# Kernel tuning notes

Hardware: AMD Instinct MI355X
Metric: run time of the kernel (lower is better)

The kernel has to match this reference:

```python
import jax, jax.numpy as jnp
import numpy as np


def setup_inputs() -> dict:
    key = jax.random.key(0)
    k1, k2, k3 = jax.random.split(key, 3)
    B, H, S, D = 4, 16, 1024, 64
    return {
        "query": jax.random.normal(k1, (B, H, S, D), dtype=jnp.float32),
        "key": jax.random.normal(k2, (B, H, D, S), dtype=jnp.float32),  # pre-transposed K
        "scale_factor": 8,  # sqrt(head_dim)
        "attention_mask": jnp.zeros((S, S), dtype=jnp.float32),
        "value": jax.random.normal(k3, (B, H, S, D), dtype=jnp.float32),
    }


def reference(query, key, scale_factor, attention_mask, value):
    # Batched equivalent of the per-(b,h) Python loop:
    # scores = Q @ K^T / scale + mask; probs = softmax(scores); out = probs @ V
    scores = jnp.matmul(query, key) / scale_factor  # [B,H,S,S]
    if attention_mask is not None:
        scores = scores + attention_mask  # broadcast [S,S] over [B,H,S,S]
    probs = jax.nn.softmax(scores, axis=-1)
    return jnp.matmul(probs, value)  # [B,H,S,D]
```

## Files before the change

kernel.cpp:

```cpp
#include <hip/hip_runtime.h>

#define BH  64
#define SEQ 1024
#define DIM 64
#define KT  64
#define NT  (SEQ / KT)

typedef __attribute__((ext_vector_type(8))) short  short8;
typedef __attribute__((ext_vector_type(4))) float  floatx4;

__device__ __forceinline__ ushort f2bf(float x) {
    union { float f; uint u; } v; v.f = x;
    uint r = v.u + 0x7FFFu + ((v.u >> 16) & 1u);
    return (ushort)(r >> 16);
}
__device__ __forceinline__ uint pack2(float lo, float hi) {
    return (uint)f2bf(lo) | ((uint)f2bf(hi) << 16);
}
__device__ __forceinline__ void gld_lds16(const void* g, void* l) {
    __builtin_amdgcn_global_load_lds(
        (const __attribute__((address_space(1))) unsigned int*)g,
        (__attribute__((address_space(3))) unsigned int*)l, 16, 0, 0);
}


__global__ __launch_bounds__(256) void prep_kv_kernel(
    const float* __restrict__ Kin,
    const float* __restrict__ Vin,
    ushort* __restrict__ Kbf, ushort* __restrict__ Vbf)
{
    __shared__ float tile[64][65];
    const int t    = threadIdx.x;
    const int head = blockIdx.y;
    const int s0   = blockIdx.x * 64;
    const int p    = t & 7;

    if (blockIdx.z == 0) {
        const float* ip = Kin + (size_t)head * DIM * SEQ;
#pragma unroll
        for (int i = 0; i < 4; ++i) {
            const int d = (t >> 4) + i * 16;
            const int c = (t & 15) * 4;
            float4 v = *(const float4*)(ip + (size_t)d * SEQ + s0 + c);
            tile[d][c]     = v.x; tile[d][c + 1] = v.y;
            tile[d][c + 2] = v.z; tile[d][c + 3] = v.w;
        }
        __syncthreads();
        char* op = (char*)(Kbf + (size_t)head * SEQ * DIM);
#pragma unroll
        for (int i = 0; i < 2; ++i) {
            const int s  = (t >> 3) + i * 32;
            const int dg = (p ^ (s & 7)) * 8;
            uint4 wv;
            wv.x = pack2(tile[dg + 0][s], tile[dg + 1][s]);
            wv.y = pack2(tile[dg + 2][s], tile[dg + 3][s]);
            wv.z = pack2(tile[dg + 4][s], tile[dg + 5][s]);
            wv.w = pack2(tile[dg + 6][s], tile[dg + 7][s]);
            *(uint4*)(op + (size_t)(s0 + s) * 128 + p * 16) = wv;
        }
    } else {
        const float* ip = Vin + (size_t)head * SEQ * DIM;
#pragma unroll
        for (int i = 0; i < 4; ++i) {
            const int ss = (t >> 4) + i * 16;
            const int c  = (t & 15) * 4;
            float4 v = *(const float4*)(ip + (size_t)(s0 + ss) * DIM + c);
            tile[ss][c]     = v.x; tile[ss][c + 1] = v.y;
            tile[ss][c + 2] = v.z; tile[ss][c + 3] = v.w;
        }
        __syncthreads();
        char* op = (char*)(Vbf + (size_t)head * SEQ * DIM) + (size_t)(s0 >> 6) * 8192;
#pragma unroll
        for (int i = 0; i < 2; ++i) {
            const int d  = (t >> 3) + i * 32;
            const int sg = (p ^ (d & 7)) * 8;
            uint4 wv;
            wv.x = pack2(tile[sg + 0][d], tile[sg + 1][d]);
            wv.y = pack2(tile[sg + 2][d], tile[sg + 3][d]);
            wv.z = pack2(tile[sg + 4][d], tile[sg + 5][d]);
            wv.w = pack2(tile[sg + 6][d], tile[sg + 7][d]);
            *(uint4*)(op + (size_t)d * 128 + p * 16) = wv;
        }
    }
}

__global__ __launch_bounds__(256, 4) void mha_mfma2_kernel(
    const float*  __restrict__ Q,
    const ushort* __restrict__ Kbf,
    const int*    __restrict__ scale_p,
    const float*  __restrict__ mask,
    const ushort* __restrict__ Vbf,
    float*        __restrict__ O)
{
    __shared__ __align__(16) ushort Ks0[KT * 64], Ks1[KT * 64];
    __shared__ __align__(16) ushort Vt0[DIM * 64], Vt1[DIM * 64];
    __shared__ __align__(16) ushort Ps[4 * 16 * 64];

    const int t    = threadIdx.x;
    const int lane = t & 63, w = t >> 6;
    const int li   = lane & 15, quad = lane >> 4;
    const int lx   = li & 7;
    const int bh   = blockIdx.x >> 4;
    const int q0   = (blockIdx.x & 15) * 64;

    const float inv_scale = 1.0f / (float)scale_p[0];

    {
        const float* Qg = Q + ((size_t)bh * SEQ + q0) * DIM;
        const int rr = t >> 4, cc = (t & 15) * 4;
#pragma unroll
        for (int i = 0; i < 4; ++i) {
            const int row = rr + 16 * i;
            float4 v = *(const float4*)(Qg + (size_t)row * DIM + cc);
            uint2 pw; pw.x = pack2(v.x, v.y); pw.y = pack2(v.z, v.w);
            *(uint2*)((char*)Ks0 + row * 128 + (((cc >> 3) ^ (row & 7)) * 16)
                      + (cc & 7) * 2) = pw;
        }
    }
    __syncthreads();
    const char* qrow = (const char*)Ks0 + (w * 16 + li) * 128;
    const short8 qa0 = *(const short8*)(qrow + ((quad ^ lx) * 16));
    const short8 qa1 = *(const short8*)(qrow + (((4 + quad) ^ lx) * 16));
    __syncthreads();

    floatx4 o[4] = {floatx4{0,0,0,0}, floatx4{0,0,0,0},
                    floatx4{0,0,0,0}, floatx4{0,0,0,0}};
    float l_r[4] = {0.f, 0.f, 0.f, 0.f};

    const char* KgH = (const char*)(Kbf + (size_t)bh * SEQ * DIM);
    const char* VgH = (const char*)(Vbf + (size_t)bh * SEQ * DIM);
    const int so = w * 2048 + lane * 16;
    char* ksd0 = (char*)Ks0 + w * 2048;
    char* ksd1 = (char*)Ks1 + w * 2048;
    char* vtd0 = (char*)Vt0 + w * 2048;
    char* vtd1 = (char*)Vt1 + w * 2048;
    char* psw  = (char*)Ps  + w * 2048;

    const float* mrow = mask + (size_t)(q0 + w * 16 + quad * 4) * SEQ + li;

    float mvc[16], mvn[16];
#pragma unroll
    for (int n = 0; n < 4; ++n)
#pragma unroll
        for (int r = 0; r < 4; ++r)
            mvc[n * 4 + r] = mrow[(size_t)r * SEQ + n * 16];
    gld_lds16(KgH + so,        ksd0);
    gld_lds16(KgH + so + 1024, ksd0 + 1024);
    gld_lds16(VgH + so,        vtd0);
    gld_lds16(VgH + so + 1024, vtd0 + 1024);
    __builtin_amdgcn_sched_barrier(0);

#pragma unroll 2
    for (int kt = 0; kt < NT; ++kt) {
        const int c = kt & 1;
        const char* ksb = c ? (const char*)Ks1 : (const char*)Ks0;
        const char* vtb = c ? (const char*)Vt1 : (const char*)Vt0;
        char* ksdN = c ? ksd0 : ksd1;
        char* vtdN = c ? vtd0 : vtd1;

        __builtin_amdgcn_s_barrier();

        const int kn = (kt + 1) & (NT - 1);
#pragma unroll
        for (int n = 0; n < 4; ++n)
#pragma unroll
            for (int r = 0; r < 4; ++r)
                mvn[n * 4 + r] = mrow[(size_t)r * SEQ + kn * KT + n * 16];
        {
            const char* kg = KgH + kn * 8192 + so;
            const char* vg = VgH + kn * 8192 + so;
            gld_lds16(kg,        ksdN);
            gld_lds16(kg + 1024, ksdN + 1024);
            gld_lds16(vg,        vtdN);
            gld_lds16(vg + 1024, vtdN + 1024);
        }
        __builtin_amdgcn_sched_barrier(0);
        asm volatile("s_waitcnt vmcnt(20)" ::: "memory");
        __builtin_amdgcn_sched_barrier(0);
        __builtin_amdgcn_s_barrier();

        floatx4 cfr[4] = {floatx4{0,0,0,0}, floatx4{0,0,0,0},
                          floatx4{0,0,0,0}, floatx4{0,0,0,0}};
        __builtin_amdgcn_s_setprio(1);
#pragma unroll
        for (int n = 0; n < 4; ++n) {
            const char* krow = ksb + (n * 16 + li) * 128;
            short8 b0 = *(const short8*)(krow + ((quad ^ lx) * 16));
            short8 b1 = *(const short8*)(krow + (((4 + quad) ^ lx) * 16));
            cfr[n] = __builtin_amdgcn_mfma_f32_16x16x32_bf16(qa0, b0, cfr[n], 0, 0, 0);
            cfr[n] = __builtin_amdgcn_mfma_f32_16x16x32_bf16(qa1, b1, cfr[n], 0, 0, 0);
        }
        __builtin_amdgcn_s_setprio(0);

#pragma unroll
        for (int n = 0; n < 4; ++n)
#pragma unroll
            for (int r = 0; r < 4; ++r) {
                float s = fminf(fmaf(cfr[n][r], inv_scale, mvc[n * 4 + r]), 80.f);
                float p = __expf(s);
                l_r[r] += p;
                const int row = quad * 4 + r, col = n * 16 + li;
                *(ushort*)(psw + row * 128 + (((col >> 3) ^ (row & 7)) * 16)
                           + (col & 7) * 2) = f2bf(p);
            }

        __builtin_amdgcn_s_setprio(1);
#pragma unroll
        for (int kk = 0; kk < 2; ++kk) {
            short8 a = *(const short8*)(psw + li * 128 + (((kk * 4 + quad) ^ lx) * 16));
#pragma unroll
            for (int n = 0; n < 4; ++n) {
                const char* vrow = vtb + (n * 16 + li) * 128;
                short8 b = *(const short8*)(vrow + (((kk * 4 + quad) ^ lx) * 16));
                o[n] = __builtin_amdgcn_mfma_f32_16x16x32_bf16(a, b, o[n], 0, 0, 0);
            }
        }
        __builtin_amdgcn_s_setprio(0);

#pragma unroll
        for (int j = 0; j < 16; ++j) mvc[j] = mvn[j];
    }

#pragma unroll
    for (int off = 1; off < 16; off <<= 1)
#pragma unroll
        for (int r = 0; r < 4; ++r)
            l_r[r] += __shfl_xor(l_r[r], off);

    float* Og = O + ((size_t)bh * SEQ + q0) * DIM;
#pragma unroll
    for (int r = 0; r < 4; ++r) {
        const float inv_l = 1.0f / l_r[r];
#pragma unroll
        for (int n = 0; n < 4; ++n)
            Og[(size_t)(w * 16 + quad * 4 + r) * DIM + n * 16 + li] = o[n][r] * inv_l;
    }
}

extern "C" void kernel_launch(void* const* d_in, const int* in_sizes, int n_in,
                              void* d_out, int out_size, void* d_ws, size_t ws_size,
                              hipStream_t stream) {
    const float* Q     = (const float*)d_in[0];
    const float* K     = (const float*)d_in[1];
    const int*   scale = (const int*)d_in[2];
    const float* mask  = (const float*)d_in[3];
    const float* V     = (const float*)d_in[4];
    float*       Out   = (float*)d_out;

    ushort* Kbf = (ushort*)d_ws;
    ushort* Vbf = Kbf + (size_t)BH * SEQ * DIM;

    prep_kv_kernel<<<dim3(SEQ / 64, BH, 2), 256, 0, stream>>>(K, V, Kbf, Vbf);
    mha_mfma2_kernel<<<dim3(BH * (SEQ / KT)), 256, 0, stream>>>(Q, Kbf, scale, mask, Vbf, Out);
}
```

Baseline: 136.3 us.

## Keep softmax probabilities in registers by computing transposed S and permuting V layout

Swaps the MFMA operands so the score tile comes out transposed, which lets each lane's exp values be packed straight into the A operand of the PV MFMA with no LDS round trip for P. The V prep kernel reorders its key groups to match this register layout, and mask loads become float4 vector loads along the key dimension. The row-sum reduction is reworked to match, and the wait count is lowered because fewer outstanding loads are issued. Bf16 rounding now uses a cheaper round-half-up perm-based pack, which changes rounding slightly on ties.

Measured after the change: 145.2 us. +6.6%, slower.

```diff
diff --git a/kernel.cpp b/kernel.cpp
--- a/kernel.cpp
+++ b/kernel.cpp
@@ -8,6 +8,7 @@
 
 typedef __attribute__((ext_vector_type(8))) short  short8;
 typedef __attribute__((ext_vector_type(4))) float  floatx4;
+typedef __attribute__((ext_vector_type(4))) uint   uintx4;
 
 __device__ __forceinline__ ushort f2bf(float x) {
     union { float f; uint u; } v; v.f = x;
@@ -16,6 +17,11 @@
 }
 __device__ __forceinline__ uint pack2(float lo, float hi) {
     return (uint)f2bf(lo) | ((uint)f2bf(hi) << 16);
+}
+__device__ __forceinline__ uint pk2(float lo, float hi) {
+    union { float f; uint u; } a, b; a.f = lo; b.f = hi;
+    uint au = a.u + 0x8000u, bu = b.u + 0x8000u;
+    return __builtin_amdgcn_perm(bu, au, 0x07060302);
 }
 __device__ __forceinline__ void gld_lds16(const void* g, void* l) {
     __builtin_amdgcn_global_load_lds(
@@ -73,12 +79,13 @@
 #pragma unroll
         for (int i = 0; i < 2; ++i) {
             const int d  = (t >> 3) + i * 32;
-            const int sg = (p ^ (d & 7)) * 8;
+            const int g  = p ^ (d & 7);
+            const int kb = ((g >> 2) * 32) + ((g & 3) * 4);
             uint4 wv;
-            wv.x = pack2(tile[sg + 0][d], tile[sg + 1][d]);
-            wv.y = pack2(tile[sg + 2][d], tile[sg + 3][d]);
-            wv.z = pack2(tile[sg + 4][d], tile[sg + 5][d]);
-            wv.w = pack2(tile[sg + 6][d], tile[sg + 7][d]);
+            wv.x = pack2(tile[kb +  0][d], tile[kb +  1][d]);
+            wv.y = pack2(tile[kb +  2][d], tile[kb +  3][d]);
+            wv.z = pack2(tile[kb + 16][d], tile[kb + 17][d]);
+            wv.w = pack2(tile[kb + 18][d], tile[kb + 19][d]);
             *(uint4*)(op + (size_t)d * 128 + p * 16) = wv;
         }
     }
@@ -94,7 +101,6 @@
 {
     __shared__ __align__(16) ushort Ks0[KT * 64], Ks1[KT * 64];
     __shared__ __align__(16) ushort Vt0[DIM * 64], Vt1[DIM * 64];
-    __shared__ __align__(16) ushort Ps[4 * 16 * 64];
 
     const int t    = threadIdx.x;
     const int lane = t & 63, w = t >> 6;
@@ -125,7 +131,7 @@
 
     floatx4 o[4] = {floatx4{0,0,0,0}, floatx4{0,0,0,0},
                     floatx4{0,0,0,0}, floatx4{0,0,0,0}};
-    float l_r[4] = {0.f, 0.f, 0.f, 0.f};
+    float l = 0.f;
 
     const char* KgH = (const char*)(Kbf + (size_t)bh * SEQ * DIM);
     const char* VgH = (const char*)(Vbf + (size_t)bh * SEQ * DIM);
@@ -134,16 +140,13 @@
     char* ksd1 = (char*)Ks1 + w * 2048;
     char* vtd0 = (char*)Vt0 + w * 2048;
     char* vtd1 = (char*)Vt1 + w * 2048;
-    char* psw  = (char*)Ps  + w * 2048;
-
-    const float* mrow = mask + (size_t)(q0 + w * 16 + quad * 4) * SEQ + li;
-
-    float mvc[16], mvn[16];
+
+    const float* mrow = mask + (size_t)(q0 + w * 16 + li) * SEQ + quad * 4;
+
+    float4 mvc[4], mvn[4];
 #pragma unroll
     for (int n = 0; n < 4; ++n)
-#pragma unroll
-        for (int r = 0; r < 4; ++r)
-            mvc[n * 4 + r] = mrow[(size_t)r * SEQ + n * 16];
+        mvc[n] = *(const float4*)(mrow + n * 16);
     gld_lds16(KgH + so,        ksd0);
     gld_lds16(KgH + so + 1024, ksd0 + 1024);
     gld_lds16(VgH + so,        vtd0);
@@ -163,9 +166,7 @@
         const int kn = (kt + 1) & (NT - 1);
 #pragma unroll
         for (int n = 0; n < 4; ++n)
-#pragma unroll
-            for (int r = 0; r < 4; ++r)
-                mvn[n * 4 + r] = mrow[(size_t)r * SEQ + kn * KT + n * 16];
+            mvn[n] = *(const float4*)(mrow + kn * KT + n * 16);
         {
             const char* kg = KgH + kn * 8192 + so;
             const char* vg = VgH + kn * 8192 + so;
@@ -175,7 +176,7 @@
             gld_lds16(vg + 1024, vtdN + 1024);
         }
         __builtin_amdgcn_sched_barrier(0);
-        asm volatile("s_waitcnt vmcnt(20)" ::: "memory");
+        asm volatile("s_waitcnt vmcnt(8)" ::: "memory");
         __builtin_amdgcn_sched_barrier(0);
         __builtin_amdgcn_s_barrier();
 
@@ -185,55 +186,58 @@
 #pragma unroll
         for (int n = 0; n < 4; ++n) {
             const char* krow = ksb + (n * 16 + li) * 128;
-            short8 b0 = *(const short8*)(krow + ((quad ^ lx) * 16));
-            short8 b1 = *(const short8*)(krow + (((4 + quad) ^ lx) * 16));
-            cfr[n] = __builtin_amdgcn_mfma_f32_16x16x32_bf16(qa0, b0, cfr[n], 0, 0, 0);
-            cfr[n] = __builtin_amdgcn_mfma_f32_16x16x32_bf16(qa1, b1, cfr[n], 0, 0, 0);
+            short8 kf0 = *(const short8*)(krow + ((quad ^ lx) * 16));
+            short8 kf1 = *(const short8*)(krow + (((4 + quad) ^ lx) * 16));
+            cfr[n] = __builtin_amdgcn_mfma_f32_16x16x32_bf16(kf0, qa0, cfr[n], 0, 0, 0);
+            cfr[n] = __builtin_amdgcn_mfma_f32_16x16x32_bf16(kf1, qa1, cfr[n], 0, 0, 0);
         }
         __builtin_amdgcn_s_setprio(0);
 
+        uint pw[8];
+#pragma unroll
+        for (int n = 0; n < 4; ++n) {
+            const float4 m4 = mvc[n];
+            float s0 = fminf(fmaf(cfr[n][0], inv_scale, m4.x), 80.f);
+            float s1 = fminf(fmaf(cfr[n][1], inv_scale, m4.y), 80.f);
+            float s2 = fminf(fmaf(cfr[n][2], inv_scale, m4.z), 80.f);
+            float s3 = fminf(fmaf(cfr[n][3], inv_scale, m4.w), 80.f);
+            float p0 = __expf(s0), p1 = __expf(s1);
+            float p2 = __expf(s2), p3 = __expf(s3);
+            l += ((p0 + p1) + (p2 + p3));
+            pw[n * 2]     = pk2(p0, p1);
+            pw[n * 2 + 1] = pk2(p2, p3);
+        }
+        const short8 pa0 = __builtin_bit_cast(short8, uintx4{pw[0], pw[1], pw[2], pw[3]});
+        const short8 pa1 = __builtin_bit_cast(short8, uintx4{pw[4], pw[5], pw[6], pw[7]});
+
+        __builtin_amdgcn_s_setprio(1);
+#pragma unroll
+        for (int n = 0; n < 4; ++n) {
+            const char* vrow = vtb + (n * 16 + li) * 128;
+            short8 b0 = *(const short8*)(vrow + ((quad ^ lx) * 16));
+            short8 b1 = *(const short8*)(vrow + (((4 + quad) ^ lx) * 16));
+            o[n] = __builtin_amdgcn_mfma_f32_16x16x32_bf16(pa0, b0, o[n], 0, 0, 0);
+            o[n] = __builtin_amdgcn_mfma_f32_16x16x32_bf16(pa1, b1, o[n], 0, 0, 0);
+        }
+        __builtin_amdgcn_s_setprio(0);
+
+#pragma unroll
+        for (int j = 0; j < 4; ++j) mvc[j] = mvn[j];
+    }
+
+    l += __shfl_xor(l, 16);
+    l += __shfl_xor(l, 32);
+    float linv[4];
+#pragma unroll
+    for (int r = 0; r < 4; ++r)
+        linv[r] = 1.0f / __shfl(l, quad * 4 + r);
+
+    float* Og = O + ((size_t)bh * SEQ + q0) * DIM;
+#pragma unroll
+    for (int r = 0; r < 4; ++r) {
 #pragma unroll
         for (int n = 0; n < 4; ++n)
-#pragma unroll
-            for (int r = 0; r < 4; ++r) {
-                float s = fminf(fmaf(cfr[n][r], inv_scale, mvc[n * 4 + r]), 80.f);
-                float p = __expf(s);
-                l_r[r] += p;
-                const int row = quad * 4 + r, col = n * 16 + li;
-                *(ushort*)(psw + row * 128 + (((col >> 3) ^ (row & 7)) * 16)
-                           + (col & 7) * 2) = f2bf(p);
-            }
-
-        __builtin_amdgcn_s_setprio(1);
-#pragma unroll
-        for (int kk = 0; kk < 2; ++kk) {
-            short8 a = *(const short8*)(psw + li * 128 + (((kk * 4 + quad) ^ lx) * 16));
-#pragma unroll
-            for (int n = 0; n < 4; ++n) {
-                const char* vrow = vtb + (n * 16 + li) * 128;
-                short8 b = *(const short8*)(vrow + (((kk * 4 + quad) ^ lx) * 16));
-                o[n] = __builtin_amdgcn_mfma_f32_16x16x32_bf16(a, b, o[n], 0, 0, 0);
-            }
-        }
-        __builtin_amdgcn_s_setprio(0);
-
-#pragma unroll
-        for (int j = 0; j < 16; ++j) mvc[j] = mvn[j];
-    }
-
-#pragma unroll
-    for (int off = 1; off < 16; off <<= 1)
-#pragma unroll
-        for (int r = 0; r < 4; ++r)
-            l_r[r] += __shfl_xor(l_r[r], off);
-
-    float* Og = O + ((size_t)bh * SEQ + q0) * DIM;
-#pragma unroll
-    for (int r = 0; r < 4; ++r) {
-        const float inv_l = 1.0f / l_r[r];
-#pragma unroll
-        for (int n = 0; n < 4; ++n)
-            Og[(size_t)(w * 16 + quad * 4 + r) * DIM + n * 16 + li] = o[n][r] * inv_l;
+            Og[(size_t)(w * 16 + quad * 4 + r) * DIM + n * 16 + li] = o[n][r] * linv[r];
     }
 }
 
```

## Split each key tile across two warps per query block with LDS reduction

Applied to the files above, without the earlier changes.

Doubles the block to 512 threads. Each pair of warps shares a 16-row query slice, and each warp of the pair handles half of every 64-key tile for both QK^T and PV. Partial outputs and row sums are combined through shared memory at the end. The aim is more waves in flight to hide latency and shorter per-warp critical paths. The cost is an extra LDS reduction, a final barrier, and fewer MFMAs per wave to amortize the per-tile synchronization.

Result: slower. 239.1 us (+75.4%).

```diff
diff --git a/kernel.cpp b/kernel.cpp
--- a/kernel.cpp
+++ b/kernel.cpp
@@ -84,7 +84,7 @@
     }
 }
 
-__global__ __launch_bounds__(256, 4) void mha_mfma2_kernel(
+__global__ __launch_bounds__(512, 8) void mha_mfma2_kernel(
     const float*  __restrict__ Q,
     const ushort* __restrict__ Kbf,
     const int*    __restrict__ scale_p,
@@ -92,12 +92,11 @@
     const ushort* __restrict__ Vbf,
     float*        __restrict__ O)
 {
-    __shared__ __align__(16) ushort Ks0[KT * 64], Ks1[KT * 64];
-    __shared__ __align__(16) ushort Vt0[DIM * 64], Vt1[DIM * 64];
-    __shared__ __align__(16) ushort Ps[4 * 16 * 64];
+    __shared__ __align__(16) char smem[40960];
 
     const int t    = threadIdx.x;
     const int lane = t & 63, w = t >> 6;
+    const int wq   = w >> 1, wk = w & 1;
     const int li   = lane & 15, quad = lane >> 4;
     const int lx   = li & 7;
     const int bh   = blockIdx.x >> 4;
@@ -109,16 +108,16 @@
         const float* Qg = Q + ((size_t)bh * SEQ + q0) * DIM;
         const int rr = t >> 4, cc = (t & 15) * 4;
 #pragma unroll
-        for (int i = 0; i < 4; ++i) {
-            const int row = rr + 16 * i;
+        for (int i = 0; i < 2; ++i) {
+            const int row = rr + 32 * i;
             float4 v = *(const float4*)(Qg + (size_t)row * DIM + cc);
             uint2 pw; pw.x = pack2(v.x, v.y); pw.y = pack2(v.z, v.w);
-            *(uint2*)((char*)Ks0 + row * 128 + (((cc >> 3) ^ (row & 7)) * 16)
+            *(uint2*)(smem + row * 128 + (((cc >> 3) ^ (row & 7)) * 16)
                       + (cc & 7) * 2) = pw;
         }
     }
     __syncthreads();
-    const char* qrow = (const char*)Ks0 + (w * 16 + li) * 128;
+    const char* qrow = smem + (wq * 16 + li) * 128;
     const short8 qa0 = *(const short8*)(qrow + ((quad ^ lx) * 16));
     const short8 qa1 = *(const short8*)(qrow + (((4 + quad) ^ lx) * 16));
     __syncthreads();
@@ -129,62 +128,49 @@
 
     const char* KgH = (const char*)(Kbf + (size_t)bh * SEQ * DIM);
     const char* VgH = (const char*)(Vbf + (size_t)bh * SEQ * DIM);
-    const int so = w * 2048 + lane * 16;
-    char* ksd0 = (char*)Ks0 + w * 2048;
-    char* ksd1 = (char*)Ks1 + w * 2048;
-    char* vtd0 = (char*)Vt0 + w * 2048;
-    char* vtd1 = (char*)Vt1 + w * 2048;
-    char* psw  = (char*)Ps  + w * 2048;
-
-    const float* mrow = mask + (size_t)(q0 + w * 16 + quad * 4) * SEQ + li;
-
-    float mvc[16], mvn[16];
-#pragma unroll
-    for (int n = 0; n < 4; ++n)
+    const int so = w * 1024 + lane * 16;
+    char* psw = smem + 32768 + w * 1024;
+
+    const float* mrow = mask + (size_t)(q0 + wq * 16 + quad * 4) * SEQ + wk * 32 + li;
+
+    float mvc[8], mvn[8];
+#pragma unroll
+    for (int n = 0; n < 2; ++n)
 #pragma unroll
         for (int r = 0; r < 4; ++r)
             mvc[n * 4 + r] = mrow[(size_t)r * SEQ + n * 16];
-    gld_lds16(KgH + so,        ksd0);
-    gld_lds16(KgH + so + 1024, ksd0 + 1024);
-    gld_lds16(VgH + so,        vtd0);
-    gld_lds16(VgH + so + 1024, vtd0 + 1024);
+    gld_lds16(KgH + so,         smem + w * 1024);
+    gld_lds16(VgH + so,         smem + 16384 + w * 1024);
     __builtin_amdgcn_sched_barrier(0);
 
 #pragma unroll 2
     for (int kt = 0; kt < NT; ++kt) {
         const int c = kt & 1;
-        const char* ksb = c ? (const char*)Ks1 : (const char*)Ks0;
-        const char* vtb = c ? (const char*)Vt1 : (const char*)Vt0;
-        char* ksdN = c ? ksd0 : ksd1;
-        char* vtdN = c ? vtd0 : vtd1;
+        const char* ksb = smem + (c ? 8192 : 0);
+        const char* vtb = smem + 16384 + (c ? 8192 : 0);
+        char* ksdN = smem + (c ? 0 : 8192) + w * 1024;
+        char* vtdN = smem + 16384 + (c ? 0 : 8192) + w * 1024;
 
         __builtin_amdgcn_s_barrier();
 
         const int kn = (kt + 1) & (NT - 1);
 #pragma unroll
-        for (int n = 0; n < 4; ++n)
+        for (int n = 0; n < 2; ++n)
 #pragma unroll
             for (int r = 0; r < 4; ++r)
                 mvn[n * 4 + r] = mrow[(size_t)r * SEQ + kn * KT + n * 16];
-        {
-            const char* kg = KgH + kn * 8192 + so;
-            const char* vg = VgH + kn * 8192 + so;
-            gld_lds16(kg,        ksdN);
-            gld_lds16(kg + 1024, ksdN + 1024);
-            gld_lds16(vg,        vtdN);
-            gld_lds16(vg + 1024, vtdN + 1024);
-        }
+        gld_lds16(KgH + kn * 8192 + so, ksdN);
+        gld_lds16(VgH + kn * 8192 + so, vtdN);
         __builtin_amdgcn_sched_barrier(0);
-        asm volatile("s_waitcnt vmcnt(20)" ::: "memory");
+        asm volatile("s_waitcnt vmcnt(10)" ::: "memory");
         __builtin_amdgcn_sched_barrier(0);
         __builtin_amdgcn_s_barrier();
 
-        floatx4 cfr[4] = {floatx4{0,0,0,0}, floatx4{0,0,0,0},
-                          floatx4{0,0,0,0}, floatx4{0,0,0,0}};
+        floatx4 cfr[2] = {floatx4{0,0,0,0}, floatx4{0,0,0,0}};
         __builtin_amdgcn_s_setprio(1);
 #pragma unroll
-        for (int n = 0; n < 4; ++n) {
-            const char* krow = ksb + (n * 16 + li) * 128;
+        for (int n = 0; n < 2; ++n) {
+            const char* krow = ksb + (wk * 32 + n * 16 + li) * 128;
             short8 b0 = *(const short8*)(krow + ((quad ^ lx) * 16));
             short8 b1 = *(const short8*)(krow + (((4 + quad) ^ lx) * 16));
             cfr[n] = __builtin_amdgcn_mfma_f32_16x16x32_bf16(qa0, b0, cfr[n], 0, 0, 0);
@@ -193,33 +179,35 @@
         __builtin_amdgcn_s_setprio(0);
 
 #pragma unroll
-        for (int n = 0; n < 4; ++n)
+        for (int n = 0; n < 2; ++n)
 #pragma unroll
             for (int r = 0; r < 4; ++r) {
                 float s = fminf(fmaf(cfr[n][r], inv_scale, mvc[n * 4 + r]), 80.f);
                 float p = __expf(s);
                 l_r[r] += p;
                 const int row = quad * 4 + r, col = n * 16 + li;
-                *(ushort*)(psw + row * 128 + (((col >> 3) ^ (row & 7)) * 16)
+                *(ushort*)(psw + row * 64 + (((col >> 3) ^ (row & 3)) * 16)
                            + (col & 7) * 2) = f2bf(p);
             }
 
         __builtin_amdgcn_s_setprio(1);
-#pragma unroll
-        for (int kk = 0; kk < 2; ++kk) {
-            short8 a = *(const short8*)(psw + li * 128 + (((kk * 4 + quad) ^ lx) * 16));
-#pragma unroll
-            for (int n = 0; n < 4; ++n) {
-                const char* vrow = vtb + (n * 16 + li) * 128;
-                short8 b = *(const short8*)(vrow + (((kk * 4 + quad) ^ lx) * 16));
-                o[n] = __builtin_amdgcn_mfma_f32_16x16x32_bf16(a, b, o[n], 0, 0, 0);
+        {
+            short8 a = *(const short8*)(psw + li * 64 + ((quad ^ (li & 3)) * 16));
+#pragma unroll
+            for (int nd = 0; nd < 4; ++nd) {
+                const char* vrow = vtb + (nd * 16 + li) * 128;
+                short8 b = *(const short8*)(vrow + (((wk * 4 + quad) ^ lx) * 16));
+                o[nd] = __builtin_amdgcn_mfma_f32_16x16x32_bf16(a, b, o[nd], 0, 0, 0);
             }
         }
         __builtin_amdgcn_s_setprio(0);
 
 #pragma unroll
-        for (int j = 0; j < 16; ++j) mvc[j] = mvn[j];
-    }
+        for (int j = 0; j < 8; ++j) mvc[j] = mvn[j];
+    }
+
+    asm volatile("s_waitcnt vmcnt(0)" ::: "memory");
+    __builtin_amdgcn_s_barrier();
 
 #pragma unroll
     for (int off = 1; off < 16; off <<= 1)
@@ -227,13 +215,37 @@
         for (int r = 0; r < 4; ++r)
             l_r[r] += __shfl_xor(l_r[r], off);
 
-    float* Og = O + ((size_t)bh * SEQ + q0) * DIM;
-#pragma unroll
-    for (int r = 0; r < 4; ++r) {
-        const float inv_l = 1.0f / l_r[r];
-#pragma unroll
-        for (int n = 0; n < 4; ++n)
-            Og[(size_t)(w * 16 + quad * 4 + r) * DIM + n * 16 + li] = o[n][r] * inv_l;
+    float* osh = (float*)smem;
+    float* lsh = (float*)(smem + 16384);
+    if (wk == 1) {
+        float* dst = osh + ((size_t)wq * 64 + lane) * 16;
+#pragma unroll
+        for (int nd = 0; nd < 4; ++nd)
+            *(floatx4*)(dst + nd * 4) = o[nd];
+        if (li == 0)
+#pragma unroll
+            for (int r = 0; r < 4; ++r)
+                lsh[wq * 16 + quad * 4 + r] = l_r[r];
+    }
+    __syncthreads();
+    if (wk == 0) {
+        const float* src = osh + ((size_t)wq * 64 + lane) * 16;
+#pragma unroll
+        for (int nd = 0; nd < 4; ++nd)
+            o[nd] += *(const floatx4*)(src + nd * 4);
+#pragma unroll
+        for (int r = 0; r < 4; ++r)
+            l_r[r] += lsh[wq * 16 + quad * 4 + r];
+
+        float* Og = O + ((size_t)bh * SEQ + q0) * DIM;
+#pragma unroll
+        for (int r = 0; r < 4; ++r) {
+            const float inv_l = 1.0f / l_r[r];
+#pragma unroll
+            for (int nd = 0; nd < 4; ++nd)
+                Og[(size_t)(wq * 16 + quad * 4 + r) * DIM + nd * 16 + li]
+                    = o[nd][r] * inv_l;
+        }
     }
 }
 
@@ -251,5 +263,5 @@
     ushort* Vbf = Kbf + (size_t)BH * SEQ * DIM;
 
     prep_kv_kernel<<<dim3(SEQ / 64, BH, 2), 256, 0, stream>>>(K, V, Kbf, Vbf);
-    mha_mfma2_kernel<<<dim3(BH * (SEQ / KT)), 256, 0, stream>>>(Q, Kbf, scale, mask, Vbf, Out);
-}
+    mha_mfma2_kernel<<<dim3(BH * (SEQ / KT)), 512, 0, stream>>>(Q, Kbf, scale, mask, Vbf, Out);
+}
```

## Use 8-wave 128-query blocks sharing K/V tiles; load Q directly to registers

Applied to the files above, without the earlier changes.

Doubles the query rows per block from 64 to 128 by using 512 threads (8 waves). All eight waves share each staged K/V tile, which halves the per-block global-to-LDS traffic per wave. Q is now loaded straight from global memory into MFMA operand registers instead of being staged through LDS, which removes two syncthreads. Launch bounds of 512 threads with min 4 blocks may tighten register limits, and the grid halves to 512 blocks.

Measured after the change: 133.3 us. 2.2% less time.

```diff
diff --git a/kernel.cpp b/kernel.cpp
--- a/kernel.cpp
+++ b/kernel.cpp
@@ -8,6 +8,7 @@
 
 typedef __attribute__((ext_vector_type(8))) short  short8;
 typedef __attribute__((ext_vector_type(4))) float  floatx4;
+typedef __attribute__((ext_vector_type(4))) uint   uintx4;
 
 __device__ __forceinline__ ushort f2bf(float x) {
     union { float f; uint u; } v; v.f = x;
@@ -84,7 +85,7 @@
     }
 }
 
-__global__ __launch_bounds__(256, 4) void mha_mfma2_kernel(
+__global__ __launch_bounds__(512, 4) void mha_mfma2_kernel(
     const float*  __restrict__ Q,
     const ushort* __restrict__ Kbf,
     const int*    __restrict__ scale_p,
@@ -94,34 +95,29 @@
 {
     __shared__ __align__(16) ushort Ks0[KT * 64], Ks1[KT * 64];
     __shared__ __align__(16) ushort Vt0[DIM * 64], Vt1[DIM * 64];
-    __shared__ __align__(16) ushort Ps[4 * 16 * 64];
+    __shared__ __align__(16) ushort Ps[8 * 16 * 64];
 
     const int t    = threadIdx.x;
     const int lane = t & 63, w = t >> 6;
     const int li   = lane & 15, quad = lane >> 4;
     const int lx   = li & 7;
-    const int bh   = blockIdx.x >> 4;
-    const int q0   = (blockIdx.x & 15) * 64;
+    const int bh   = blockIdx.x >> 3;
+    const int q0   = (blockIdx.x & 7) * 128;
 
     const float inv_scale = 1.0f / (float)scale_p[0];
 
+    short8 qa0, qa1;
     {
-        const float* Qg = Q + ((size_t)bh * SEQ + q0) * DIM;
-        const int rr = t >> 4, cc = (t & 15) * 4;
-#pragma unroll
-        for (int i = 0; i < 4; ++i) {
-            const int row = rr + 16 * i;
-            float4 v = *(const float4*)(Qg + (size_t)row * DIM + cc);
-            uint2 pw; pw.x = pack2(v.x, v.y); pw.y = pack2(v.z, v.w);
-            *(uint2*)((char*)Ks0 + row * 128 + (((cc >> 3) ^ (row & 7)) * 16)
-                      + (cc & 7) * 2) = pw;
-        }
-    }
-    __syncthreads();
-    const char* qrow = (const char*)Ks0 + (w * 16 + li) * 128;
-    const short8 qa0 = *(const short8*)(qrow + ((quad ^ lx) * 16));
-    const short8 qa1 = *(const short8*)(qrow + (((4 + quad) ^ lx) * 16));
-    __syncthreads();
+        const float* Qr = Q + ((size_t)bh * SEQ + q0 + w * 16 + li) * DIM + quad * 8;
+        float4 a = *(const float4*)(Qr);
+        float4 b = *(const float4*)(Qr + 4);
+        float4 c = *(const float4*)(Qr + 32);
+        float4 d = *(const float4*)(Qr + 36);
+        qa0 = __builtin_bit_cast(short8,
+              uintx4{pack2(a.x, a.y), pack2(a.z, a.w), pack2(b.x, b.y), pack2(b.z, b.w)});
+        qa1 = __builtin_bit_cast(short8,
+              uintx4{pack2(c.x, c.y), pack2(c.z, c.w), pack2(d.x, d.y), pack2(d.z, d.w)});
+    }
 
     floatx4 o[4] = {floatx4{0,0,0,0}, floatx4{0,0,0,0},
                     floatx4{0,0,0,0}, floatx4{0,0,0,0}};
@@ -129,11 +125,11 @@
 
     const char* KgH = (const char*)(Kbf + (size_t)bh * SEQ * DIM);
     const char* VgH = (const char*)(Vbf + (size_t)bh * SEQ * DIM);
-    const int so = w * 2048 + lane * 16;
-    char* ksd0 = (char*)Ks0 + w * 2048;
-    char* ksd1 = (char*)Ks1 + w * 2048;
-    char* vtd0 = (char*)Vt0 + w * 2048;
-    char* vtd1 = (char*)Vt1 + w * 2048;
+    const int so = w * 1024 + lane * 16;
+    char* ksd0 = (char*)Ks0 + w * 1024;
+    char* ksd1 = (char*)Ks1 + w * 1024;
+    char* vtd0 = (char*)Vt0 + w * 1024;
+    char* vtd1 = (char*)Vt1 + w * 1024;
     char* psw  = (char*)Ps  + w * 2048;
 
     const float* mrow = mask + (size_t)(q0 + w * 16 + quad * 4) * SEQ + li;
@@ -144,10 +140,8 @@
 #pragma unroll
         for (int r = 0; r < 4; ++r)
             mvc[n * 4 + r] = mrow[(size_t)r * SEQ + n * 16];
-    gld_lds16(KgH + so,        ksd0);
-    gld_lds16(KgH + so + 1024, ksd0 + 1024);
-    gld_lds16(VgH + so,        vtd0);
-    gld_lds16(VgH + so + 1024, vtd0 + 1024);
+    gld_lds16(KgH + so, ksd0);
+    gld_lds16(VgH + so, vtd0);
     __builtin_amdgcn_sched_barrier(0);
 
 #pragma unroll 2
@@ -166,16 +160,10 @@
 #pragma unroll
             for (int r = 0; r < 4; ++r)
                 mvn[n * 4 + r] = mrow[(size_t)r * SEQ + kn * KT + n * 16];
-        {
-            const char* kg = KgH + kn * 8192 + so;
-            const char* vg = VgH + kn * 8192 + so;
-            gld_lds16(kg,        ksdN);
-            gld_lds16(kg + 1024, ksdN + 1024);
-            gld_lds16(vg,        vtdN);
-            gld_lds16(vg + 1024, vtdN + 1024);
-        }
+        gld_lds16(KgH + kn * 8192 + so, ksdN);
+        gld_lds16(VgH + kn * 8192 + so, vtdN);
         __builtin_amdgcn_sched_barrier(0);
-        asm volatile("s_waitcnt vmcnt(20)" ::: "memory");
+        asm volatile("s_waitcnt vmcnt(18)" ::: "memory");
         __builtin_amdgcn_sched_barrier(0);
         __builtin_amdgcn_s_barrier();
 
@@ -251,5 +239,5 @@
     ushort* Vbf = Kbf + (size_t)BH * SEQ * DIM;
 
     prep_kv_kernel<<<dim3(SEQ / 64, BH, 2), 256, 0, stream>>>(K, V, Kbf, Vbf);
-    mha_mfma2_kernel<<<dim3(BH * (SEQ / KT)), 256, 0, stream>>>(Q, Kbf, scale, mask, Vbf, Out);
-}
+    mha_mfma2_kernel<<<dim3(BH * (SEQ / 128)), 512, 0, stream>>>(Q, Kbf, scale, mask, Vbf, Out);
+}
```
